# Performance work log

Hardware: AMD Instinct MI355X
Metric: run time of the kernel (lower is better)

The kernel has to match this reference:

```python
import jax, jax.numpy as jnp
import numpy as np

D_MODEL = 1024
NHEAD = 16
HEAD_DIM = D_MODEL // NHEAD
HID = int(D_MODEL * 4.0 * (2.0 / 3.0))  # 2730, matches int(d_model*mlp_ratio*2/3)
EPS = 1e-5


def setup_inputs() -> dict:
    key = jax.random.key(0)
    ks = jax.random.split(key, 12)
    s = lambda fi, fo: (2.0 / (fi + fo)) ** 0.5
    inp = {
        "x": jax.random.normal(ks[0], (2, 2048, D_MODEL), dtype=jnp.float32),
        "ln1_w": jnp.ones((D_MODEL,), jnp.float32),
        "ln1_b": jnp.zeros((D_MODEL,), jnp.float32),
        "wq": jax.random.normal(ks[1], (D_MODEL, D_MODEL), jnp.float32) * s(D_MODEL, D_MODEL),
        "wk": jax.random.normal(ks[2], (D_MODEL, D_MODEL), jnp.float32) * s(D_MODEL, D_MODEL),
        "wv": jax.random.normal(ks[3], (D_MODEL, D_MODEL), jnp.float32) * s(D_MODEL, D_MODEL),
        "wg": jax.random.normal(ks[4], (D_MODEL, D_MODEL), jnp.float32) * s(D_MODEL, D_MODEL),
        "wo": jax.random.normal(ks[5], (D_MODEL, D_MODEL), jnp.float32) * s(D_MODEL, D_MODEL),
        "ln2_w": jnp.ones((D_MODEL,), jnp.float32),
        "ln2_b": jnp.zeros((D_MODEL,), jnp.float32),
        "w_in": jax.random.normal(ks[6], (D_MODEL, 2 * HID), jnp.float32) * s(D_MODEL, 2 * HID),
        "b_in": jnp.zeros((2 * HID,), jnp.float32),
        "w_out": jax.random.normal(ks[7], (HID, D_MODEL), jnp.float32) * s(HID, D_MODEL),
        "b_out": jnp.zeros((D_MODEL,), jnp.float32),
    }
    return inp


def _layernorm(x, w, b):
    mu = jnp.mean(x, axis=-1, keepdims=True)
    var = jnp.var(x, axis=-1, keepdims=True)
    return (x - mu) * jax.lax.rsqrt(var + EPS) * w + b


def _decay_matrix(S):
    # gamma_h = 1 - 2^{-5-h}, RetNet multiscale decays
    gamma = 1.0 - jnp.exp2(-5.0 - jnp.arange(NHEAD, dtype=jnp.float32))  # [H]
    n = jnp.arange(S, dtype=jnp.float32)
    exp = n[:, None] - n[None, :]                     # [S, S]
    mask = exp >= 0
    d = gamma[:, None, None] ** jnp.where(mask, exp, 0.0)  # [H, S, S]
    return jnp.where(mask[None], d, 0.0)


def _msr(xn, wq, wk, wv, wg, wo):
    B, S, _ = xn.shape
    split = lambda t: t.reshape(B, S, NHEAD, HEAD_DIM).transpose(0, 2, 1, 3)  # bhsd
    q = split(xn @ wq) * (HEAD_DIM ** -0.5)
    k = split(xn @ wk)
    v = split(xn @ wv)
    Dm = _decay_matrix(S)                                   # [H, S, S]
    scores = jnp.einsum("bhsd,bhtd->bhst", q, k) * Dm[None]  # causal decayed retention
    out = jnp.einsum("bhst,bhtd->bhsd", scores, v)
    # per-head normalization (GroupNorm over head dim, no affine)
    mu = jnp.mean(out, axis=-1, keepdims=True)
    var = jnp.var(out, axis=-1, keepdims=True)
    out = (out - mu) * jax.lax.rsqrt(var + 1e-6)
    out = out.transpose(0, 2, 1, 3).reshape(B, S, D_MODEL)
    out = out * jax.nn.silu(xn @ wg)                        # swish gate
    return out @ wo


def _swiglu(x, w_in, b_in, w_out, b_out):
    ab = x @ w_in + b_in
    a, b = ab[..., :HID], ab[..., HID:]
    return (a * jax.nn.silu(b)) @ w_out + b_out


def reference(x, ln1_w, ln1_b, wq, wk, wv, wg, wo, ln2_w, ln2_b, w_in, b_in, w_out, b_out):
    h = _msr(_layernorm(x, ln1_w, ln1_b), wq, wk, wv, wg, wo)
    x = x + h  # dropout/drop_path identity at eval
    x = x + _swiglu(_layernorm(x, ln2_w, ln2_b), w_in, b_in, w_out, b_out)
    return x
```

## Files before the change

kernel.cpp:

```cpp
#include <hip/hip_runtime.h>
#include <math.h>

#define D_MODEL 1024
#define NHEAD   16
#define HDIM    64
#define HID     2730
#define HID_PAD 2816
#define SEQ     2048
#define BATCH   2
#define NTOK    (BATCH * SEQ)
#define QKG     3072

typedef __attribute__((ext_vector_type(8))) short bf16x8;
typedef __attribute__((ext_vector_type(4))) float f32x4;
typedef __attribute__((ext_vector_type(4))) short s16x4;

static __device__ inline short f2bf(float f)
{
    union { float f; unsigned int u; } c; c.f = f;
    unsigned int r = c.u + 0x7FFFu + ((c.u >> 16) & 1u);
    return (short)(r >> 16);
}
static __device__ inline float bf2f(short s)
{
    union { unsigned int u; float f; } c;
    c.u = ((unsigned int)(unsigned short)s) << 16;
    return c.f;
}

#define GLD16(gsrc, ldst) \
    __builtin_amdgcn_global_load_lds((const __attribute__((address_space(1))) void*)(gsrc), \
                                     (__attribute__((address_space(3))) void*)(ldst), 16, 0, 0)

__global__ void ln_kernel(const float* __restrict__ x,
                          const float* __restrict__ w,
                          const float* __restrict__ b,
                          short* __restrict__ out,
                          float eps)
{
    int row = blockIdx.x;
    int t = threadIdx.x;
    const float4* xr = (const float4*)(x + (size_t)row * D_MODEL);
    float4 v = xr[t];
    float s  = v.x + v.y + v.z + v.w;
    float sq = v.x * v.x + v.y * v.y + v.z * v.z + v.w * v.w;
#pragma unroll
    for (int off = 32; off > 0; off >>= 1) {
        s  += __shfl_xor(s, off);
        sq += __shfl_xor(sq, off);
    }
    __shared__ float ss[4], ssq[4];
    int wave = t >> 6;
    if ((t & 63) == 0) { ss[wave] = s; ssq[wave] = sq; }
    __syncthreads();
    s  = ss[0] + ss[1] + ss[2] + ss[3];
    sq = ssq[0] + ssq[1] + ssq[2] + ssq[3];
    float mu  = s * (1.0f / D_MODEL);
    float var = sq * (1.0f / D_MODEL) - mu * mu;
    float inv = rsqrtf(var + eps);
    float4 wv = ((const float4*)w)[t];
    float4 bv = ((const float4*)b)[t];
    s16x4 o;
    o.x = f2bf((v.x - mu) * inv * wv.x + bv.x);
    o.y = f2bf((v.y - mu) * inv * wv.y + bv.y);
    o.z = f2bf((v.z - mu) * inv * wv.z + bv.z);
    o.w = f2bf((v.w - mu) * inv * wv.w + bv.w);
    *(s16x4*)(out + (size_t)row * D_MODEL + 4 * t) = o;
}

struct TJob {
    const float* src;
    short* dst;
    int ldsrc, coloff, nvalid, kvalid, KPAD, NPAD;
};
struct TJobs { TJob j[8]; };

__global__ __launch_bounds__(256) void transpose_all(TJobs jobs)
{
    TJob jb = jobs.j[blockIdx.z];
    int k0 = blockIdx.x * 64, n0 = blockIdx.y * 64;
    if (k0 >= jb.KPAD || n0 >= jb.NPAD) return;
    __shared__ float tile[64][65];
    int t = threadIdx.x;
    {
        int kk = t >> 2, np = (t & 3) << 4;
        int k = k0 + kk;
        bool kok = k < jb.kvalid;
        const float* srow = jb.src + (size_t)k * jb.ldsrc + jb.coloff + n0 + np;
#pragma unroll
        for (int i = 0; i < 16; ++i) {
            int n = n0 + np + i;
            tile[kk][np + i] = (kok && n < jb.nvalid) ? srow[i] : 0.0f;
        }
    }
    __syncthreads();
    {
        int nn = t >> 2, kp = (t & 3) << 4;
        short* drow = jb.dst + (size_t)(n0 + nn) * jb.KPAD + k0 + kp;
#pragma unroll
        for (int v4 = 0; v4 < 4; ++v4) {
            s16x4 o;
            o.x = f2bf(tile[kp + v4 * 4 + 0][nn]);
            o.y = f2bf(tile[kp + v4 * 4 + 1][nn]);
            o.z = f2bf(tile[kp + v4 * 4 + 2][nn]);
            o.w = f2bf(tile[kp + v4 * 4 + 3][nn]);
            *(s16x4*)(drow + v4 * 4) = o;
        }
    }
}

template<int EPI>
static __device__ __forceinline__ void gemm_core(
        const short* __restrict__ A, int lda,
        const short* __restrict__ Bt,
        const float* __restrict__ bias,
        const float* __restrict__ R, int ldr,
        void* __restrict__ C, int ldc, int K, int bm, int bn,
        short (*As)[4096], short (*Bs)[4096])
{
    int t = threadIdx.x;
    int w = t >> 6;
    int lane = t & 63;
    int quad = lane >> 4;
    int l15  = lane & 15;

    const short* gA0 = A  + (size_t)(bm + (t >> 2)) * lda + ((t & 3) << 3);
    const short* gA1 = gA0 + (size_t)64 * lda;
    const short* gB0 = Bt + (size_t)(bn + (t >> 2)) * K + ((t & 3) << 3);
    const short* gB1 = gB0 + (size_t)64 * K;
    int wb = w << 9;

    int wr = (w >> 1) * 64;
    int wc = (w & 1) * 64;

    f32x4 acc[4][4];
#pragma unroll
    for (int i = 0; i < 4; ++i)
#pragma unroll
        for (int j = 0; j < 4; ++j) acc[i][j] = (f32x4){0.f, 0.f, 0.f, 0.f};

    GLD16(gA0, &As[0][wb]);
    GLD16(gA1, &As[0][2048 + wb]);
    GLD16(gB0, &Bs[0][wb]);
    GLD16(gB1, &Bs[0][2048 + wb]);

    for (int k0 = 0; k0 < K; k0 += 32) {
        int cur = (k0 >> 5) & 1;
        __syncthreads();
        int k1 = k0 + 32;
        if (k1 < K) {
            GLD16(gA0 + k1, &As[cur ^ 1][wb]);
            GLD16(gA1 + k1, &As[cur ^ 1][2048 + wb]);
            GLD16(gB0 + k1, &Bs[cur ^ 1][wb]);
            GLD16(gB1 + k1, &Bs[cur ^ 1][2048 + wb]);
        }
        bf16x8 af[4], bfr[4];
#pragma unroll
        for (int i = 0; i < 4; ++i)
            af[i] = *(const bf16x8*)(&As[cur][(wr + i * 16 + l15) * 32 + quad * 8]);
#pragma unroll
        for (int j = 0; j < 4; ++j)
            bfr[j] = *(const bf16x8*)(&Bs[cur][(wc + j * 16 + l15) * 32 + quad * 8]);
#pragma unroll
        for (int i = 0; i < 4; ++i)
#pragma unroll
            for (int j = 0; j < 4; ++j)
                acc[i][j] = __builtin_amdgcn_mfma_f32_16x16x32_bf16(af[i], bfr[j], acc[i][j], 0, 0, 0);
    }

#pragma unroll
    for (int i = 0; i < 4; ++i) {
        int gr = bm + wr + i * 16 + quad * 4;
#pragma unroll
        for (int j = 0; j < 4; ++j) {
            int gc = bn + wc + j * 16 + l15;
#pragma unroll
            for (int r = 0; r < 4; ++r) {
                float val = acc[i][j][r];
                size_t idx = (size_t)(gr + r) * ldc + gc;
                if (EPI == 0) {
                    ((short*)C)[idx] = f2bf(val);
                } else if (EPI == 1) {
                    ((float*)C)[idx] = val + R[(size_t)(gr + r) * ldr + gc];
                } else {
                    ((float*)C)[idx] = val + bias[gc] + R[(size_t)(gr + r) * ldr + gc];
                }
            }
        }
    }
}

__global__ __launch_bounds__(256, 4) void proj_kernel(
        const short* __restrict__ xn,
        const short* __restrict__ qkgT,
        short* __restrict__ qkg,
        const short* __restrict__ wvT,
        short* __restrict__ vT)
{
    __shared__ short As[2][4096];
    __shared__ short Bs[2][4096];
    int id = blockIdx.x;
    if (id < 768) {
        int bm = (id & 31) * 128, bn = (id >> 5) * 128;
        gemm_core<0>(xn, D_MODEL, qkgT, nullptr, nullptr, 0, qkg, QKG, D_MODEL, bm, bn, As, Bs);
    } else {
        int i2 = id - 768;
        int bn = (i2 & 31) * 128, bm = (i2 >> 5) * 128;
        gemm_core<0>(wvT, D_MODEL, xn, nullptr, nullptr, 0, vT, NTOK, D_MODEL, bm, bn, As, Bs);
    }
}

template<int EPI>
__global__ __launch_bounds__(256, 4) void gemm_n64(
        const short* __restrict__ A, int lda,
        const short* __restrict__ Bt,
        const float* __restrict__ bias,
        const float* __restrict__ R, int ldr,
        void* __restrict__ C, int ldc, int K)
{
    __shared__ short As[2][4096];
    __shared__ short Bs[2][2048];
    int bm = blockIdx.x * 128;
    int bn = blockIdx.y * 64;
    int t = threadIdx.x;
    int w = t >> 6;
    int lane = t & 63;
    int quad = lane >> 4;
    int l15  = lane & 15;

    const short* gA0 = A  + (size_t)(bm + (t >> 2)) * lda + ((t & 3) << 3);
    const short* gA1 = gA0 + (size_t)64 * lda;
    const short* gB0 = Bt + (size_t)(bn + (t >> 2)) * K + ((t & 3) << 3);
    int wb = w << 9;

    int wr = (w >> 1) * 64;
    int wc = (w & 1) * 32;

    f32x4 acc[4][2];
#pragma unroll
    for (int i = 0; i < 4; ++i)
#pragma unroll
        for (int j = 0; j < 2; ++j) acc[i][j] = (f32x4){0.f, 0.f, 0.f, 0.f};

    GLD16(gA0, &As[0][wb]);
    GLD16(gA1, &As[0][2048 + wb]);
    GLD16(gB0, &Bs[0][wb]);

    for (int k0 = 0; k0 < K; k0 += 32) {
        int cur = (k0 >> 5) & 1;
        __syncthreads();
        int k1 = k0 + 32;
        if (k1 < K) {
            GLD16(gA0 + k1, &As[cur ^ 1][wb]);
            GLD16(gA1 + k1, &As[cur ^ 1][2048 + wb]);
            GLD16(gB0 + k1, &Bs[cur ^ 1][wb]);
        }
        bf16x8 af[4], bfr[2];
#pragma unroll
        for (int i = 0; i < 4; ++i)
            af[i] = *(const bf16x8*)(&As[cur][(wr + i * 16 + l15) * 32 + quad * 8]);
#pragma unroll
        for (int j = 0; j < 2; ++j)
            bfr[j] = *(const bf16x8*)(&Bs[cur][(wc + j * 16 + l15) * 32 + quad * 8]);
#pragma unroll
        for (int i = 0; i < 4; ++i)
#pragma unroll
            for (int j = 0; j < 2; ++j)
                acc[i][j] = __builtin_amdgcn_mfma_f32_16x16x32_bf16(af[i], bfr[j], acc[i][j], 0, 0, 0);
    }

#pragma unroll
    for (int i = 0; i < 4; ++i) {
        int gr = bm + wr + i * 16 + quad * 4;
#pragma unroll
        for (int j = 0; j < 2; ++j) {
            int gc = bn + wc + j * 16 + l15;
#pragma unroll
            for (int r = 0; r < 4; ++r) {
                float val = acc[i][j][r];
                size_t idx = (size_t)(gr + r) * ldc + gc;
                if (EPI == 0) {
                    ((short*)C)[idx] = f2bf(val);
                } else if (EPI == 1) {
                    ((float*)C)[idx] = val + R[(size_t)(gr + r) * ldr + gc];
                } else {
                    ((float*)C)[idx] = val + bias[gc] + R[(size_t)(gr + r) * ldr + gc];
                }
            }
        }
    }
}

__global__ __launch_bounds__(256, 4) void mlp_fused(
        const short* __restrict__ A,
        const short* __restrict__ w_inT,
        const float* __restrict__ b_in,
        short* __restrict__ hm)
{
    __shared__ short As[2][4096];
    __shared__ short Ba[2][2048];
    __shared__ short Bb[2][2048];
    const int K = D_MODEL;
    int bm = blockIdx.x * 128;
    int bn = blockIdx.y * 64;
    int t = threadIdx.x;
    int w = t >> 6;
    int lane = t & 63;
    int quad = lane >> 4;
    int l15  = lane & 15;

    const short* gA0 = A + (size_t)(bm + (t >> 2)) * K + ((t & 3) << 3);
    const short* gA1 = gA0 + (size_t)64 * K;
    const short* gBa = w_inT + (size_t)(bn + (t >> 2)) * K + ((t & 3) << 3);
    const short* gBb = gBa + (size_t)HID_PAD * K;
    int wb = w << 9;

    int wr = (w >> 1) * 64;
    int wc = (w & 1) * 32;

    f32x4 acca[4][2], accb[4][2];
#pragma unroll
    for (int i = 0; i < 4; ++i)
#pragma unroll
        for (int j = 0; j < 2; ++j) {
            acca[i][j] = (f32x4){0.f, 0.f, 0.f, 0.f};
            accb[i][j] = (f32x4){0.f, 0.f, 0.f, 0.f};
        }

    GLD16(gA0, &As[0][wb]);
    GLD16(gA1, &As[0][2048 + wb]);
    GLD16(gBa, &Ba[0][wb]);
    GLD16(gBb, &Bb[0][wb]);

    for (int k0 = 0; k0 < K; k0 += 32) {
        int cur = (k0 >> 5) & 1;
        __syncthreads();
        int k1 = k0 + 32;
        if (k1 < K) {
            GLD16(gA0 + k1, &As[cur ^ 1][wb]);
            GLD16(gA1 + k1, &As[cur ^ 1][2048 + wb]);
            GLD16(gBa + k1, &Ba[cur ^ 1][wb]);
            GLD16(gBb + k1, &Bb[cur ^ 1][wb]);
        }
        bf16x8 af[4], baf[2], bbf[2];
#pragma unroll
        for (int i = 0; i < 4; ++i)
            af[i] = *(const bf16x8*)(&As[cur][(wr + i * 16 + l15) * 32 + quad * 8]);
#pragma unroll
        for (int j = 0; j < 2; ++j) {
            baf[j] = *(const bf16x8*)(&Ba[cur][(wc + j * 16 + l15) * 32 + quad * 8]);
            bbf[j] = *(const bf16x8*)(&Bb[cur][(wc + j * 16 + l15) * 32 + quad * 8]);
        }
#pragma unroll
        for (int i = 0; i < 4; ++i)
#pragma unroll
            for (int j = 0; j < 2; ++j) {
                acca[i][j] = __builtin_amdgcn_mfma_f32_16x16x32_bf16(af[i], baf[j], acca[i][j], 0, 0, 0);
                accb[i][j] = __builtin_amdgcn_mfma_f32_16x16x32_bf16(af[i], bbf[j], accb[i][j], 0, 0, 0);
            }
    }

#pragma unroll
    for (int i = 0; i < 4; ++i) {
        int gr = bm + wr + i * 16 + quad * 4;
#pragma unroll
        for (int j = 0; j < 2; ++j) {
            int gc = bn + wc + j * 16 + l15;
            bool ok = gc < HID;
            float ba = ok ? b_in[gc] : 0.0f;
            float bb = ok ? b_in[HID + gc] : 0.0f;
#pragma unroll
            for (int r = 0; r < 4; ++r) {
                float a  = acca[i][j][r] + ba;
                float bv = accb[i][j][r] + bb;
                float val = ok ? a * (bv / (1.0f + expf(-bv))) : 0.0f;
                hm[(size_t)(gr + r) * HID_PAD + gc] = f2bf(val);
            }
        }
    }
}

#define PSTR 72

__global__ __launch_bounds__(512) void retention_mfma(
        const short* __restrict__ qkg,
        const short* __restrict__ vT,
        short* __restrict__ rg)
{
    int qb = (int)gridDim.x - 1 - (int)blockIdx.x;
    int h  = blockIdx.y;
    int b  = blockIdx.z;

    __shared__ short ks[2][4096];
    __shared__ short vt[2][4096];
    __shared__ short ps[8][16 * PSTR];

    int tid  = threadIdx.x;
    int w    = tid >> 6;
    int lane = tid & 63;
    int quad = lane >> 4;
    int l15  = lane & 15;

    float log2g = log1pf(-exp2f(-5.0f - (float)h)) * 1.4426950408889634f;
    int hcol = h * HDIM;
    int s0 = qb * 128;
    size_t tok0 = (size_t)b * SEQ;

    int sch  = tid >> 8;
    int srow = (tid >> 2) & 63;
    int sp8  = (tid & 3) << 3;
    const short* kbase  = qkg + (tok0 + srow) * QKG + 1024 + hcol + sch * 32 + sp8;
    const short* vtbase = vT + (size_t)(hcol + srow) * NTOK + tok0 + sch * 32 + sp8;
    int lb = tid << 3;

    const short* qrow = qkg + (tok0 + s0 + w * 16 + l15) * QKG + hcol;
    bf16x8 qa0 = *(const bf16x8*)(qrow + quad * 8);
    bf16x8 qa1 = *(const bf16x8*)(qrow + 32 + quad * 8);

    float colfac[4];
#pragma unroll
    for (int tile = 0; tile < 4; ++tile)
        colfac[tile] = exp2f(-(float)(tile * 16 + l15) * log2g) * 0.125f;

    f32x4 oacc[4];
#pragma unroll
    for (int i = 0; i < 4; ++i) oacc[i] = (f32x4){0.f, 0.f, 0.f, 0.f};

    int sbase = s0 + w * 16 + quad * 4;
    int tmax = 2 * qb + 1;

    GLD16(kbase, &ks[0][lb]);
    GLD16(vtbase, &vt[0][lb]);

    for (int tb = 0; tb <= tmax; ++tb) {
        int cur = tb & 1;
        __syncthreads();
        if (tb < tmax) {
            GLD16(kbase + (size_t)(tb + 1) * 64 * QKG, &ks[cur ^ 1][lb]);
            GLD16(vtbase + (tb + 1) * 64, &vt[cur ^ 1][lb]);
        }

        f32x4 sacc[4];
#pragma unroll
        for (int i = 0; i < 4; ++i) sacc[i] = (f32x4){0.f, 0.f, 0.f, 0.f};
#pragma unroll
        for (int tile = 0; tile < 4; ++tile) {
            bf16x8 kb0 = *(const bf16x8*)(&ks[cur][(tile * 16 + l15) * 32 + quad * 8]);
            bf16x8 kb1 = *(const bf16x8*)(&ks[cur][2048 + (tile * 16 + l15) * 32 + quad * 8]);
            sacc[tile] = __builtin_amdgcn_mfma_f32_16x16x32_bf16(qa0, kb0, sacc[tile], 0, 0, 0);
            sacc[tile] = __builtin_amdgcn_mfma_f32_16x16x32_bf16(qa1, kb1, sacc[tile], 0, 0, 0);
        }

        int fbi = sbase - tb * 64;
        float rf[4];
#pragma unroll
        for (int reg = 0; reg < 4; ++reg)
            rf[reg] = exp2f((float)(fbi + reg) * log2g);

        if (tb * 64 + 63 > s0 + w * 16) {
#pragma unroll
            for (int tile = 0; tile < 4; ++tile) {
                int tt = tile * 16 + l15;
#pragma unroll
                for (int reg = 0; reg < 4; ++reg) {
                    float p = (fbi + reg >= tt) ? sacc[tile][reg] * rf[reg] * colfac[tile] : 0.0f;
                    ps[w][(quad * 4 + reg) * PSTR + tile * 16 + l15] = f2bf(p);
                }
            }
        } else {
#pragma unroll
            for (int tile = 0; tile < 4; ++tile)
#pragma unroll
                for (int reg = 0; reg < 4; ++reg)
                    ps[w][(quad * 4 + reg) * PSTR + tile * 16 + l15] =
                        f2bf(sacc[tile][reg] * (rf[reg] * colfac[tile]));
        }

#pragma unroll
        for (int ksi = 0; ksi < 2; ++ksi) {
            bf16x8 pa = *(const bf16x8*)(&ps[w][l15 * PSTR + ksi * 32 + quad * 8]);
#pragma unroll
            for (int dt = 0; dt < 4; ++dt) {
                bf16x8 vb = *(const bf16x8*)(&vt[cur][ksi * 2048 + (dt * 16 + l15) * 32 + quad * 8]);
                oacc[dt] = __builtin_amdgcn_mfma_f32_16x16x32_bf16(pa, vb, oacc[dt], 0, 0, 0);
            }
        }
    }

    float s1[4], s2[4];
#pragma unroll
    for (int reg = 0; reg < 4; ++reg) {
        s1[reg] = oacc[0][reg] + oacc[1][reg] + oacc[2][reg] + oacc[3][reg];
        s2[reg] = oacc[0][reg] * oacc[0][reg] + oacc[1][reg] * oacc[1][reg]
                + oacc[2][reg] * oacc[2][reg] + oacc[3][reg] * oacc[3][reg];
    }
#pragma unroll
    for (int off = 1; off < 16; off <<= 1) {
#pragma unroll
        for (int reg = 0; reg < 4; ++reg) {
            s1[reg] += __shfl_xor(s1[reg], off);
            s2[reg] += __shfl_xor(s2[reg], off);
        }
    }
    size_t rowtok = tok0 + s0 + w * 16 + quad * 4;
    short* obase = rg + rowtok * D_MODEL + hcol;
    const short* gbase = qkg + rowtok * QKG + 2048 + hcol;
#pragma unroll
    for (int reg = 0; reg < 4; ++reg) {
        float mu  = s1[reg] * (1.0f / 64.0f);
        float var = s2[reg] * (1.0f / 64.0f) - mu * mu;
        float inv = rsqrtf(var + 1e-6f);
#pragma unroll
        for (int dt = 0; dt < 4; ++dt) {
            float gv = bf2f(gbase[(size_t)reg * QKG + dt * 16 + l15]);
            float val = (oacc[dt][reg] - mu) * inv * (gv / (1.0f + expf(-gv)));
            obase[(size_t)reg * D_MODEL + dt * 16 + l15] = f2bf(val);
        }
    }
}

extern "C" void kernel_launch(void* const* d_in, const int* in_sizes, int n_in,
                              void* d_out, int out_size, void* d_ws, size_t ws_size,
                              hipStream_t stream)
{
    const float* x     = (const float*)d_in[0];
    const float* ln1w  = (const float*)d_in[1];
    const float* ln1b  = (const float*)d_in[2];
    const float* wq    = (const float*)d_in[3];
    const float* wk    = (const float*)d_in[4];
    const float* wv    = (const float*)d_in[5];
    const float* wg    = (const float*)d_in[6];
    const float* wo    = (const float*)d_in[7];
    const float* ln2w  = (const float*)d_in[8];
    const float* ln2b  = (const float*)d_in[9];
    const float* w_in  = (const float*)d_in[10];
    const float* b_in  = (const float*)d_in[11];
    const float* w_out = (const float*)d_in[12];
    const float* b_out = (const float*)d_in[13];
    float* out = (float*)d_out;
    char* base = (char*)d_ws;

    const size_t MB = 1u << 20;
    short* xn     = (short*)(base);
    short* qkgT   = (short*)(base +  8 * MB);
    short* wvT    = (short*)(base + 14 * MB);
    short* woT    = (short*)(base + 16 * MB);
    short* w_inT  = (short*)(base + 18 * MB);
    short* w_outT = (short*)(base + 29 * MB);
    short* qkg    = (short*)(base + 35 * MB);
    short* hm     = (short*)(base + 35 * MB);
    short* vT     = (short*)(base + 59 * MB);
    short* rg     = (short*)(base + 67 * MB);

    TJobs jobs;
    jobs.j[0] = { wq,    qkgT,                          1024,    0, 1024, 1024, 1024, 1024 };
    jobs.j[1] = { wk,    qkgT + 1024 * 1024,            1024,    0, 1024, 1024, 1024, 1024 };
    jobs.j[2] = { wg,    qkgT + 2 * 1024 * 1024,        1024,    0, 1024, 1024, 1024, 1024 };
    jobs.j[3] = { wv,    wvT,                           1024,    0, 1024, 1024, 1024, 1024 };
    jobs.j[4] = { wo,    woT,                           1024,    0, 1024, 1024, 1024, 1024 };
    jobs.j[5] = { w_in,  w_inT,                         2 * HID, 0,   HID, 1024, 1024, HID_PAD };
    jobs.j[6] = { w_in,  w_inT + (size_t)HID_PAD * 1024, 2 * HID, HID, HID, 1024, 1024, HID_PAD };
    jobs.j[7] = { w_out, w_outT,                        1024,    0, 1024, HID, HID_PAD, 1024 };
    transpose_all<<<dim3(44, 44, 8), 256, 0, stream>>>(jobs);

    ln_kernel<<<NTOK, 256, 0, stream>>>(x, ln1w, ln1b, xn, 1e-5f);
    proj_kernel<<<1024, 256, 0, stream>>>(xn, qkgT, qkg, wvT, vT);
    retention_mfma<<<dim3(SEQ / 128, NHEAD, BATCH), 512, 0, stream>>>(qkg, vT, rg);
    gemm_n64<1><<<dim3(32, 16), 256, 0, stream>>>(rg, D_MODEL, woT, nullptr, x, D_MODEL, out, D_MODEL, D_MODEL);
    ln_kernel<<<NTOK, 256, 0, stream>>>(out, ln2w, ln2b, xn, 1e-5f);
    mlp_fused<<<dim3(NTOK / 128, HID_PAD / 64), 256, 0, stream>>>(xn, w_inT, b_in, hm);
    gemm_n64<2><<<dim3(32, 16), 256, 0, stream>>>(hm, HID_PAD, w_outT, b_out, out, D_MODEL, out, D_MODEL, HID_PAD);
}
```

Baseline: 414.2 us.

## Rewrite fused SwiGLU up-projection GEMM with 256x256 tiles and phased pipelining

The mlp_fused kernel moves from 128x64 (x2 gate/value) tiles with 256 threads and K-step 32 to 256x128 (x2) tiles with 512 threads and K-step 64. Shared memory gets an XOR swizzle to avoid bank conflicts, and the loads are pipelined in four phases with raw s_barrier, explicit vmcnt waits and s_setprio around the MFMA bursts. The aim is more reuse per tile loaded into shared memory and better overlap of global loads with matrix math. In exchange it uses 128KB of shared memory per block, far more registers, and fewer blocks (16x22 grid), which may hurt occupancy and load balance.

After: 427.0 us. 1.03x slower.

```diff
diff --git a/kernel.cpp b/kernel.cpp
--- a/kernel.cpp
+++ b/kernel.cpp
@@ -291,90 +291,137 @@
     }
 }
 
-__global__ __launch_bounds__(256, 4) void mlp_fused(
+#define SB   __builtin_amdgcn_s_barrier()
+
+#define STG_A(s, c0, c1, koff) do { \
+    GLD16(pA + (size_t)(c0) * 1024 + (koff), &As[s][(c0) * 64 + (w << 9)]); \
+    GLD16(pA + (size_t)(c1) * 1024 + (koff), &As[s][(c1) * 64 + (w << 9)]); } while (0)
+
+#define STG_B(s, c0, c1, koff) do { \
+    GLD16(pB[(c0) >> 6] + (koff), &Bs[s][(c0) * 64 + (w << 9)]); \
+    GLD16(pB[(c1) >> 6] + (koff), &Bs[s][(c1) * 64 + (w << 9)]); } while (0)
+
+#define LDA_F(S, FM, KK) \
+    (*(const bf16x8*)(&As[S][(wr * 128 + (FM) * 16 + l15) * 64 + ((((KK) << 2) | quad) ^ r3) * 8]))
+#define LDB_F(S, N, KK) \
+    (*(const bf16x8*)(&Bs[S][((N) * 64 + wcw * 16 + l15) * 64 + ((((KK) << 2) | quad) ^ r3) * 8]))
+
+#define RD_A(S, MH) do { _Pragma("unroll") \
+    for (int m_ = 0; m_ < 4; ++m_) { af[m_][0] = LDA_F(S, (MH) * 4 + m_, 0); \
+                                     af[m_][1] = LDA_F(S, (MH) * 4 + m_, 1); } } while (0)
+#define RD_B(S, NH) do { _Pragma("unroll") \
+    for (int n_ = 0; n_ < 2; ++n_) { bfv[(NH) * 2 + n_][0] = LDB_F(S, (NH) * 2 + n_, 0); \
+                                     bfv[(NH) * 2 + n_][1] = LDB_F(S, (NH) * 2 + n_, 1); } } while (0)
+
+#define QUAD(MH, NH) do { _Pragma("unroll") \
+    for (int m_ = 0; m_ < 4; ++m_) { _Pragma("unroll") \
+        for (int n_ = 0; n_ < 2; ++n_) { \
+            acc[(MH) * 4 + m_][(NH) * 2 + n_] = __builtin_amdgcn_mfma_f32_16x16x32_bf16( \
+                af[m_][0], bfv[(NH) * 2 + n_][0], acc[(MH) * 4 + m_][(NH) * 2 + n_], 0, 0, 0); \
+            acc[(MH) * 4 + m_][(NH) * 2 + n_] = __builtin_amdgcn_mfma_f32_16x16x32_bf16( \
+                af[m_][1], bfv[(NH) * 2 + n_][1], acc[(MH) * 4 + m_][(NH) * 2 + n_], 0, 0, 0); \
+        } } } while (0)
+
+#define PH_MID do { SB; asm volatile("s_waitcnt lgkmcnt(0)"); \
+                    __builtin_amdgcn_s_setprio(1); } while (0)
+#define PH_END do { __builtin_amdgcn_s_setprio(0); SB; } while (0)
+
+__global__ __launch_bounds__(512, 2) void mlp_fused(
         const short* __restrict__ A,
         const short* __restrict__ w_inT,
         const float* __restrict__ b_in,
         short* __restrict__ hm)
 {
-    __shared__ short As[2][4096];
-    __shared__ short Ba[2][2048];
-    __shared__ short Bb[2][2048];
-    const int K = D_MODEL;
-    int bm = blockIdx.x * 128;
-    int bn = blockIdx.y * 64;
-    int t = threadIdx.x;
-    int w = t >> 6;
-    int lane = t & 63;
-    int quad = lane >> 4;
-    int l15  = lane & 15;
-
-    const short* gA0 = A + (size_t)(bm + (t >> 2)) * K + ((t & 3) << 3);
-    const short* gA1 = gA0 + (size_t)64 * K;
-    const short* gBa = w_inT + (size_t)(bn + (t >> 2)) * K + ((t & 3) << 3);
-    const short* gBb = gBa + (size_t)HID_PAD * K;
-    int wb = w << 9;
-
-    int wr = (w >> 1) * 64;
-    int wc = (w & 1) * 32;
-
-    f32x4 acca[4][2], accb[4][2];
-#pragma unroll
-    for (int i = 0; i < 4; ++i)
+    __shared__ short As[2][16384];
+    __shared__ short Bs[2][16384];
+
+    const int bm  = blockIdx.x * 256;
+    const int bn0 = blockIdx.y * 128;
+    const int t = threadIdx.x;
+    const int w = t >> 6, lane = t & 63, quad = lane >> 4, l15 = lane & 15;
+    const int wr = w >> 2;
+    const int wcw = w & 3;
+    const int r3 = l15 & 7;
+
+    const int srow = t >> 3;
+    const int go = (t & 7) ^ (srow & 7);
+    const short* pA = A + (size_t)(bm + srow) * 1024 + go * 8;
+    const int wc_ = (srow >> 4) & 3, ii = srow & 15;
+    const short* pB[4];
+#pragma unroll
+    for (int c = 0; c < 4; ++c) {
+        int wrow = ((c & 1) ? HID_PAD : 0) + bn0 + (c >> 1) * 64 + wc_ * 16 + ii;
+        pB[c] = w_inT + (size_t)wrow * 1024 + go * 8;
+    }
+
+    f32x4 acc[8][4];
+#pragma unroll
+    for (int i = 0; i < 8; ++i)
+#pragma unroll
+        for (int j = 0; j < 4; ++j) acc[i][j] = (f32x4){0.f, 0.f, 0.f, 0.f};
+
+    STG_A(0, 0, 128, 0);
+    STG_A(0, 64, 192, 0);
+    STG_B(0, 0, 64, 0);
+    STG_B(0, 128, 192, 0);
+    STG_A(1, 0, 128, 64);
+    STG_B(1, 0, 64, 64);
+    STG_B(1, 128, 192, 64);
+    asm volatile("s_waitcnt vmcnt(6)");
+    SB;
+
+#pragma unroll 1
+    for (int it = 0; it < 8; ++it) {
+        const int kb = it * 128;
+        const bool more = (it < 7);
+        bf16x8 af[4][2], bfv[4][2];
+
+        RD_A(0, 0); RD_B(0, 0);
+        STG_A(1, 64, 192, kb + 64);
+        PH_MID; QUAD(0, 0); PH_END;
+        RD_B(0, 1);
+        if (more) STG_A(0, 0, 128, kb + 128);
+        PH_MID; QUAD(0, 1); PH_END;
+        RD_A(0, 1);
+        if (more) STG_B(0, 0, 64, kb + 128);
+        PH_MID; QUAD(1, 0); PH_END;
+        if (more) STG_B(0, 128, 192, kb + 128);
+        PH_MID; QUAD(1, 1);
+        __builtin_amdgcn_s_setprio(0);
+        if (more) { asm volatile("s_waitcnt vmcnt(6)"); }
+        else      { asm volatile("s_waitcnt vmcnt(0)"); }
+        SB;
+        RD_A(1, 0); RD_B(1, 0);
+        if (more) STG_A(0, 64, 192, kb + 128);
+        PH_MID; QUAD(0, 0); PH_END;
+        RD_B(1, 1);
+        if (more) STG_A(1, 0, 128, kb + 192);
+        PH_MID; QUAD(0, 1); PH_END;
+        RD_A(1, 1);
+        if (more) STG_B(1, 0, 64, kb + 192);
+        PH_MID; QUAD(1, 0); PH_END;
+        if (more) STG_B(1, 128, 192, kb + 192);
+        PH_MID; QUAD(1, 1);
+        __builtin_amdgcn_s_setprio(0);
+        if (more) { asm volatile("s_waitcnt vmcnt(6)"); }
+        SB;
+    }
+
+#pragma unroll
+    for (int m = 0; m < 8; ++m) {
+        int row = bm + wr * 128 + m * 16 + quad * 4;
 #pragma unroll
         for (int j = 0; j < 2; ++j) {
-            acca[i][j] = (f32x4){0.f, 0.f, 0.f, 0.f};
-            accb[i][j] = (f32x4){0.f, 0.f, 0.f, 0.f};
-        }
-
-    GLD16(gA0, &As[0][wb]);
-    GLD16(gA1, &As[0][2048 + wb]);
-    GLD16(gBa, &Ba[0][wb]);
-    GLD16(gBb, &Bb[0][wb]);
-
-    for (int k0 = 0; k0 < K; k0 += 32) {
-        int cur = (k0 >> 5) & 1;
-        __syncthreads();
-        int k1 = k0 + 32;
-        if (k1 < K) {
-            GLD16(gA0 + k1, &As[cur ^ 1][wb]);
-            GLD16(gA1 + k1, &As[cur ^ 1][2048 + wb]);
-            GLD16(gBa + k1, &Ba[cur ^ 1][wb]);
-            GLD16(gBb + k1, &Bb[cur ^ 1][wb]);
-        }
-        bf16x8 af[4], baf[2], bbf[2];
-#pragma unroll
-        for (int i = 0; i < 4; ++i)
-            af[i] = *(const bf16x8*)(&As[cur][(wr + i * 16 + l15) * 32 + quad * 8]);
-#pragma unroll
-        for (int j = 0; j < 2; ++j) {
-            baf[j] = *(const bf16x8*)(&Ba[cur][(wc + j * 16 + l15) * 32 + quad * 8]);
-            bbf[j] = *(const bf16x8*)(&Bb[cur][(wc + j * 16 + l15) * 32 + quad * 8]);
-        }
-#pragma unroll
-        for (int i = 0; i < 4; ++i)
-#pragma unroll
-            for (int j = 0; j < 2; ++j) {
-                acca[i][j] = __builtin_amdgcn_mfma_f32_16x16x32_bf16(af[i], baf[j], acca[i][j], 0, 0, 0);
-                accb[i][j] = __builtin_amdgcn_mfma_f32_16x16x32_bf16(af[i], bbf[j], accb[i][j], 0, 0, 0);
-            }
-    }
-
-#pragma unroll
-    for (int i = 0; i < 4; ++i) {
-        int gr = bm + wr + i * 16 + quad * 4;
-#pragma unroll
-        for (int j = 0; j < 2; ++j) {
-            int gc = bn + wc + j * 16 + l15;
-            bool ok = gc < HID;
-            float ba = ok ? b_in[gc] : 0.0f;
-            float bb = ok ? b_in[HID + gc] : 0.0f;
+            int col = bn0 + j * 64 + wcw * 16 + l15;
+            bool ok = col < HID;
+            float ba = ok ? b_in[col] : 0.0f;
+            float bb = ok ? b_in[HID + col] : 0.0f;
 #pragma unroll
             for (int r = 0; r < 4; ++r) {
-                float a  = acca[i][j][r] + ba;
-                float bv = accb[i][j][r] + bb;
+                float a  = acc[m][2 * j][r] + ba;
+                float bv = acc[m][2 * j + 1][r] + bb;
                 float val = ok ? a * (bv / (1.0f + expf(-bv))) : 0.0f;
-                hm[(size_t)(gr + r) * HID_PAD + gc] = f2bf(val);
+                hm[(size_t)(row + r) * HID_PAD + col] = f2bf(val);
             }
         }
     }
@@ -568,6 +615,6 @@
     retention_mfma<<<dim3(SEQ / 128, NHEAD, BATCH), 512, 0, stream>>>(qkg, vT, rg);
     gemm_n64<1><<<dim3(32, 16), 256, 0, stream>>>(rg, D_MODEL, woT, nullptr, x, D_MODEL, out, D_MODEL, D_MODEL);
     ln_kernel<<<NTOK, 256, 0, stream>>>(out, ln2w, ln2b, xn, 1e-5f);
-    mlp_fused<<<dim3(NTOK / 128, HID_PAD / 64), 256, 0, stream>>>(xn, w_inT, b_in, hm);
+    mlp_fused<<<dim3(NTOK / 256, HID_PAD / 128), 512, 0, stream>>>(xn, w_inT, b_in, hm);
     gemm_n64<2><<<dim3(32, 16), 256, 0, stream>>>(hm, HID_PAD, w_outT, b_out, out, D_MODEL, out, D_MODEL, HID_PAD);
 }
```
